# Kernel optimization log

Hardware: AMD Instinct MI355X
Metric: run time of the kernel (lower is better)

## Reference

```python
import jax, jax.numpy as jnp
import numpy as np

NUM_GROUPS = 14
GROUP_IN = 9
SHARED_H = 16
SHARED_OUT = 4
SALE_DIM = 1
FINAL_H = 128
ACTION_DIM = 15


def setup_inputs() -> dict:
    key = jax.random.key(0)
    ks = jax.random.split(key, 10)
    B = 262144
    features_2 = jax.random.normal(ks[0], (B, NUM_GROUPS * GROUP_IN), dtype=jnp.float32)
    sale_predictions = jax.random.normal(ks[1], (B, SALE_DIM), dtype=jnp.float32)
    # shared block params (one block, shared across all 14 groups)
    W1 = jax.random.normal(ks[2], (GROUP_IN, SHARED_H), dtype=jnp.float32) / np.sqrt(GROUP_IN)
    b1 = jnp.zeros((SHARED_H,), dtype=jnp.float32)
    W2 = jax.random.normal(ks[3], (SHARED_H, SHARED_OUT), dtype=jnp.float32) / np.sqrt(SHARED_H)
    b2 = jnp.zeros((SHARED_OUT,), dtype=jnp.float32)
    # final block params
    fin_in = SHARED_OUT * NUM_GROUPS + SALE_DIM  # 57
    W3 = jax.random.normal(ks[4], (fin_in, FINAL_H), dtype=jnp.float32) / np.sqrt(fin_in)
    b3 = jnp.zeros((FINAL_H,), dtype=jnp.float32)
    W4 = jax.random.normal(ks[5], (FINAL_H, ACTION_DIM * 2), dtype=jnp.float32) / np.sqrt(FINAL_H)
    b4 = jnp.zeros((ACTION_DIM * 2,), dtype=jnp.float32)
    return {"features_2": features_2, "sale_predictions": sale_predictions,
            "W1": W1, "b1": b1, "W2": W2, "b2": b2,
            "W3": W3, "b3": b3, "W4": W4, "b4": b4}


def reference(features_2, sale_predictions, W1, b1, W2, b2, W3, b3, W4, b4):
    B = features_2.shape[0]
    # [B, 14, 9]: all 14 groups through the SAME shared block, batched as one GEMM
    g = features_2.reshape(B, NUM_GROUPS, GROUP_IN)
    h = jax.nn.relu(jnp.einsum('bgi,ih->bgh', g, W1) + b1)          # [B,14,16]
    s = jax.nn.relu(jnp.einsum('bgh,ho->bgo', h, W2) + b2)          # [B,14,4]
    shared_outputs = s.reshape(B, NUM_GROUPS * SHARED_OUT)          # [B,56]
    combined = jnp.concatenate([shared_outputs, sale_predictions], axis=1)  # [B,57]
    z = jax.nn.relu(combined @ W3 + b3)                             # [B,128]
    out = z @ W4 + b4                                               # [B,30]
    action_mean, action_log_std = jnp.split(out, 2, axis=1)
    action_mean = jnp.tanh(action_mean)
    action_std = jnp.exp(action_log_std)
    return (action_mean, action_std)
```

## Files before the change

kernel.cpp:

```cpp
#include <hip/hip_runtime.h>


typedef float f4v  __attribute__((ext_vector_type(4)));
typedef short s8v  __attribute__((ext_vector_type(8)));
typedef _Float16 h8v __attribute__((ext_vector_type(8)));
typedef unsigned u2v __attribute__((ext_vector_type(2)));
typedef unsigned u4v __attribute__((ext_vector_type(4)));

constexpr int NG = 14, GI = 9, FH = 128, AD = 15;
constexpr int SLICE = 7712;

__device__ __forceinline__ unsigned short f2bf(float f) {
    unsigned u = __builtin_bit_cast(unsigned, f);
    return (unsigned short)((u + 0x7fffu + ((u >> 16) & 1u)) >> 16);
}
__device__ __forceinline__ float bf2f(unsigned short h) {
    return __builtin_bit_cast(float, (unsigned)h << 16);
}
__device__ __forceinline__ f4v load4u(const float* p) {
    f4v v; __builtin_memcpy(&v, p, 16); return v;
}
__device__ __forceinline__ unsigned pkh(float a, float b) {
    return __builtin_bit_cast(unsigned, __builtin_amdgcn_cvt_pkrtz(a, b));
}
__device__ __forceinline__ unsigned pkbf(float a, float b) {
    unsigned r;
    asm("v_cvt_pk_bf16_f32 %0, %1, %2" : "=v"(r) : "v"(a), "v"(b));
    return r;
}

__global__ void pack_kernel(const float* __restrict__ W3,
                            const float* __restrict__ W4,
                            const float* __restrict__ W1,
                            const float* __restrict__ W2,
                            unsigned short* __restrict__ pk) {
    unsigned short* W3h = pk;
    unsigned short* W3l = pk + 8192;
    unsigned short* W4h = pk + 16384;
    unsigned short* W4l = pk + 20480;
    int t = blockIdx.x * 256 + threadIdx.x;
    if (t < 8192) {
        int j = t & 7, l = (t >> 3) & 63, nt = (t >> 9) & 7, kt = t >> 12;
        int k = kt * 32 + (l >> 4) * 8 + j, n = nt * 16 + (l & 15);
        float v = (k < 57) ? W3[k * FH + n] : 0.f;
        unsigned short h = f2bf(v);
        W3h[t] = h;
        W3l[t] = f2bf(v - bf2f(h));
    }
    if (t < 4096) {
        int j = t & 7, l = (t >> 3) & 63, nt = (t >> 9) & 1, kt = t >> 10;
        int k = kt * 32 + (l >> 4) * 8 + j, n = nt * 16 + (l & 15);
        float v = (n < 30) ? W4[k * 30 + n] : 0.f;
        unsigned short h = f2bf(v);
        W4h[t] = h;
        W4l[t] = f2bf(v - bf2f(h));
    }
    if (t < 512) {
        int l = t >> 3, j = t & 7;
        int p = l >> 4, m = l & 15;
        int k = (j < 4) ? (p * 4 + j) : (16 + p * 4 + (j - 4));
        float v1 = (k < GI) ? W1[k * 16 + m] : 0.f;
        float v2 = (k < 16 && m < 4) ? W2[k * 4 + m] : 0.f;
        _Float16 h1 = (_Float16)v1, h2 = (_Float16)v2;
        pk[24576 + t] = __builtin_bit_cast(unsigned short, h1);
        pk[25088 + t] = __builtin_bit_cast(unsigned short, h2);
    }
}

__global__ __launch_bounds__(256, 4) void actor_fused(
    const float* __restrict__ x,
    const float* __restrict__ sale,
    const float* __restrict__ b1,
    const float* __restrict__ b2,
    const float* __restrict__ b3,
    const float* __restrict__ b4,
    const unsigned short* __restrict__ pk,
    float* __restrict__ om, float* __restrict__ os)
{
    __shared__ unsigned short xz[11552];
    __shared__ unsigned short sh[4096];

    const int tid  = threadIdx.x;
    const int wv   = __builtin_amdgcn_readfirstlane(tid >> 6);
    const int lane = tid & 63;
    const int row0 = blockIdx.x * 64;
    const int p    = lane >> 4;
    const int col  = lane & 15;

    {
        const float* xw0 = x + (size_t)(row0 + 16 * wv) * (NG * GI);
        #pragma unroll
        for (int i = 0; i < 4; ++i) {
            int unit = i * 64 + lane;
            if (i < 3 || lane < 32) {
                int rl = (unit * 149797) >> 21;
                int g  = unit - rl * 14;
                const float* xs = xw0 + rl * 126 + g * 9;
                f4v a = load4u(xs);
                f4v b = load4u(xs + 4);
                float c = xs[8];
                int bo = (16 * wv + rl) * 120 + g * 8;
                *(u2v*)((char*)xz + bo) = (u2v){pkh(a[0], a[1]), pkh(a[2], a[3])};
                *(u2v*)((char*)xz + SLICE + bo) = (u2v){pkh(b[0], b[1]), pkh(b[2], b[3])};
                *(u2v*)((char*)xz + 2 * SLICE + bo) = (u2v){pkh(c, 0.f), 0u};
            }
        }
    }
    if (lane < 16) {
        int r = 16 * wv + lane;
        float sv = sale[row0 + r];
        int byt = (r * 128 + 112) ^ ((r & 7) << 4);
        *(unsigned short*)((char*)sh + byt) = f2bf(sv);
        #pragma unroll
        for (int kk = 57; kk < 64; ++kk) {
            int bb = (r * 128 + kk * 2) ^ ((r & 7) << 4);
            *(unsigned short*)((char*)sh + bb) = 0;
        }
    }

    const int r1 = 16 * wv + col;
    const h8v w1t = __builtin_bit_cast(h8v, *(const s8v*)(pk + 24576 + lane * 8));
    const h8v w2t = __builtin_bit_cast(h8v, *(const s8v*)(pk + 25088 + lane * 8));
    const f4v b1f = load4u(b1 + p * 4);
    const f4v b2f = load4u(b2);
    const int psl = (p < 2) ? p : 2;
    const char* xb8 = (char*)xz + psl * SLICE + r1 * 120;
    const int sbase = r1 * 128;
    const int ssw   = (r1 & 7) << 4;

    #pragma unroll
    for (int g = 0; g < NG; ++g) {
        u2v d = *(const u2v*)(xb8 + g * 8);
        h8v xb = __builtin_bit_cast(h8v, (u4v){d[0], d[1], 0u, 0u});
        f4v ha = __builtin_amdgcn_mfma_f32_16x16x32_f16(w1t, xb, b1f, 0, 0, 0);
        float h0 = fmaxf(ha[0], 0.f), h1 = fmaxf(ha[1], 0.f);
        float h2 = fmaxf(ha[2], 0.f), h3 = fmaxf(ha[3], 0.f);
        h8v hb = __builtin_bit_cast(h8v, (u4v){pkh(h0, h1), pkh(h2, h3), 0u, 0u});
        f4v sa = __builtin_amdgcn_mfma_f32_16x16x32_f16(w2t, hb, b2f, 0, 0, 0);
        float s0 = fmaxf(sa[0], 0.f), s1 = fmaxf(sa[1], 0.f);
        float s2 = fmaxf(sa[2], 0.f), s3 = fmaxf(sa[3], 0.f);
        unsigned q0 = pkbf(s0, s1), q1 = pkbf(s2, s3);
        if (p == 0) {
            int byt = (sbase + g * 8) ^ ssw;
            *(u2v*)((char*)sh + byt) = (u2v){q0, q1};
        }
    }

    __syncthreads();

    const s8v* W3hv = (const s8v*)pk;
    const s8v* W3lv = (const s8v*)(pk + 8192);
    s8v bh[2][2], bl[2][2];
    #pragma unroll
    for (int kt = 0; kt < 2; ++kt)
        #pragma unroll
        for (int ntl = 0; ntl < 2; ++ntl) {
            int nt = 2 * wv + ntl;
            bh[kt][ntl] = W3hv[(kt * 8 + nt) * 64 + lane];
            bl[kt][ntl] = W3lv[(kt * 8 + nt) * 64 + lane];
        }
    f4v acc[4][2];
    #pragma unroll
    for (int ntl = 0; ntl < 2; ++ntl) {
        float bv = b3[32 * wv + ntl * 16 + col];
        #pragma unroll
        for (int mt = 0; mt < 4; ++mt) acc[mt][ntl] = (f4v){bv, bv, bv, bv};
    }
    #pragma unroll
    for (int kt = 0; kt < 2; ++kt) {
        s8v ah[4];
        #pragma unroll
        for (int mt = 0; mt < 4; ++mt) {
            int rr = mt * 16 + col;
            int byt = (rr * 128 + kt * 64 + p * 16) ^ ((rr & 7) << 4);
            ah[mt] = *(const s8v*)((char*)sh + byt);
        }
        #pragma unroll
        for (int mt = 0; mt < 4; ++mt)
            #pragma unroll
            for (int ntl = 0; ntl < 2; ++ntl) {
                acc[mt][ntl] = __builtin_amdgcn_mfma_f32_16x16x32_bf16(ah[mt], bh[kt][ntl], acc[mt][ntl], 0, 0, 0);
                acc[mt][ntl] = __builtin_amdgcn_mfma_f32_16x16x32_bf16(ah[mt], bl[kt][ntl], acc[mt][ntl], 0, 0, 0);
            }
    }
    #pragma unroll
    for (int mt = 0; mt < 4; ++mt)
        #pragma unroll
        for (int ntl = 0; ntl < 2; ++ntl) {
            int kk  = ntl * 16 + col;
            int tau = (kk & 4) ? 4 + (kk >> 3) : (kk >> 3);
            int eidx = mt * 2048 + wv * 512 + tau * 64 + (kk & 3) * 16 + (p << 2);
            float v0 = fmaxf(acc[mt][ntl][0], 0.f);
            float v1 = fmaxf(acc[mt][ntl][1], 0.f);
            float v2 = fmaxf(acc[mt][ntl][2], 0.f);
            float v3 = fmaxf(acc[mt][ntl][3], 0.f);
            *(u2v*)(xz + eidx) = (u2v){pkbf(v0, v1), pkbf(v2, v3)};
        }

    __syncthreads();

    const s8v* W4hv = (const s8v*)(pk + 16384);
    const s8v* W4lv = (const s8v*)(pk + 20480);
    const int mq   = __builtin_amdgcn_readfirstlane(wv >> 1);
    const int nq   = __builtin_amdgcn_readfirstlane(wv & 1);
    const int ocol = nq * 16 + col;
    const float b4i = (ocol < 30) ? b4[ocol] : 0.f;

    s8v wh[4], wl[4];
    #pragma unroll
    for (int kt = 0; kt < 4; ++kt) {
        wh[kt] = W4hv[(kt * 2 + nq) * 64 + lane];
        wl[kt] = W4lv[(kt * 2 + nq) * 64 + lane];
    }
    unsigned base = (unsigned)(size_t)&xz[0] + (unsigned)(2 * mq) * 4096u
                  + (unsigned)(lane * 8);
    u2v f0[4][2], f1[4][2];
    #pragma unroll
    for (int c = 0; c < 4; ++c) {
        unsigned a0 = base + c * 1024;
        unsigned a1 = a0 + 4096;
        asm volatile("ds_read_b64_tr_b16 %0, %1" : "=v"(f0[c][0]) : "v"(a0));
        asm volatile("ds_read_b64_tr_b16 %0, %1 offset:512" : "=v"(f0[c][1]) : "v"(a0));
        asm volatile("ds_read_b64_tr_b16 %0, %1" : "=v"(f1[c][0]) : "v"(a1));
        asm volatile("ds_read_b64_tr_b16 %0, %1 offset:512" : "=v"(f1[c][1]) : "v"(a1));
    }
    asm volatile("s_waitcnt lgkmcnt(0)" ::: "memory");
    __builtin_amdgcn_sched_barrier(0);

    f4v oa0 = (f4v){b4i, b4i, b4i, b4i};
    f4v oa1 = oa0;
    #pragma unroll
    for (int kt = 0; kt < 4; ++kt) {
        s8v z0 = __builtin_bit_cast(s8v,
            (u4v){f0[kt][0][0], f0[kt][0][1], f0[kt][1][0], f0[kt][1][1]});
        s8v z1 = __builtin_bit_cast(s8v,
            (u4v){f1[kt][0][0], f1[kt][0][1], f1[kt][1][0], f1[kt][1][1]});
        oa0 = __builtin_amdgcn_mfma_f32_16x16x32_bf16(z0, wh[kt], oa0, 0, 0, 0);
        oa0 = __builtin_amdgcn_mfma_f32_16x16x32_bf16(z0, wl[kt], oa0, 0, 0, 0);
        oa1 = __builtin_amdgcn_mfma_f32_16x16x32_bf16(z1, wh[kt], oa1, 0, 0, 0);
        oa1 = __builtin_amdgcn_mfma_f32_16x16x32_bf16(z1, wl[kt], oa1, 0, 0, 0);
    }
    #pragma unroll
    for (int mi = 0; mi < 2; ++mi) {
        f4v oa = mi ? oa1 : oa0;
        #pragma unroll
        for (int i = 0; i < 4; ++i) {
            int grow = row0 + mq * 32 + mi * 16 + p * 4 + i;
            float v = oa[i];
            if (ocol < AD) {
                float tc = fminf(fmaxf(v, -20.f), 20.f);
                float e = __expf(2.f * tc);
                om[(size_t)grow * AD + ocol] = (e - 1.f) / (e + 1.f);
            } else if (ocol < 2 * AD) {
                os[(size_t)grow * AD + (ocol - AD)] = __expf(v);
            }
        }
    }
}

extern "C" void kernel_launch(void* const* d_in, const int* in_sizes, int n_in,
                              void* d_out, int out_size, void* d_ws, size_t ws_size,
                              hipStream_t stream) {
    const float* x    = (const float*)d_in[0];
    const float* sale = (const float*)d_in[1];
    const float* W1   = (const float*)d_in[2];
    const float* b1   = (const float*)d_in[3];
    const float* W2   = (const float*)d_in[4];
    const float* b2   = (const float*)d_in[5];
    const float* W3   = (const float*)d_in[6];
    const float* b3   = (const float*)d_in[7];
    const float* W4   = (const float*)d_in[8];
    const float* b4   = (const float*)d_in[9];

    int B = in_sizes[1];
    float* om = (float*)d_out;
    float* os = om + (size_t)B * AD;
    unsigned short* pk = (unsigned short*)d_ws;

    pack_kernel<<<32, 256, 0, stream>>>(W3, W4, W1, W2, pk);
    actor_fused<<<B / 64, 256, 0, stream>>>(x, sale, b1, b2, b3, b4,
                                            pk, om, os);
}
```

Measured before the change: 49.37 us.

## Compact ninth input feature into a small LDS slice and hoist weight loads

The ninth feature of each group is now stored as a single fp16 in a compact LDS region and packed into the third dword of the MFMA B operand. W1 is repacked so that k=8 lands in the p=0 lane slot. This shrinks LDS from about 23KB to about 17.5KB per block, which may raise occupancy, and removes the padded third-slice writes. W3/b3 and W4/b4 global loads are hoisted earlier so they overlap with the input staging and the first GEMM, at the cost of more live registers.

```diff
diff --git a/kernel.cpp b/kernel.cpp
--- a/kernel.cpp
+++ b/kernel.cpp
@@ -9,6 +9,7 @@
 
 constexpr int NG = 14, GI = 9, FH = 128, AD = 15;
 constexpr int SLICE = 7712;
+constexpr int S2OFF = 15424;
 
 __device__ __forceinline__ unsigned short f2bf(float f) {
     unsigned u = __builtin_bit_cast(unsigned, f);
@@ -58,9 +59,12 @@
     if (t < 512) {
         int l = t >> 3, j = t & 7;
         int p = l >> 4, m = l & 15;
-        int k = (j < 4) ? (p * 4 + j) : (16 + p * 4 + (j - 4));
-        float v1 = (k < GI) ? W1[k * 16 + m] : 0.f;
-        float v2 = (k < 16 && m < 4) ? W2[k * 4 + m] : 0.f;
+        float v1 = 0.f;
+        if (p == 0 && j < 4)       v1 = W1[j * 16 + m];
+        else if (p == 0 && j == 4) v1 = W1[8 * 16 + m];
+        else if (p == 1 && j < 4)  v1 = W1[(4 + j) * 16 + m];
+        int k2 = (j < 4) ? (p * 4 + j) : 99;
+        float v2 = (k2 < 16 && m < 4) ? W2[k2 * 4 + m] : 0.f;
         _Float16 h1 = (_Float16)v1, h2 = (_Float16)v2;
         pk[24576 + t] = __builtin_bit_cast(unsigned short, h1);
         pk[25088 + t] = __builtin_bit_cast(unsigned short, h2);
@@ -77,7 +81,7 @@
     const unsigned short* __restrict__ pk,
     float* __restrict__ om, float* __restrict__ os)
 {
-    __shared__ unsigned short xz[11552];
+    __shared__ unsigned short xz[8736];
     __shared__ unsigned short sh[4096];
 
     const int tid  = threadIdx.x;
@@ -86,6 +90,20 @@
     const int row0 = blockIdx.x * 64;
     const int p    = lane >> 4;
     const int col  = lane & 15;
+
+    const s8v* W3hv = (const s8v*)pk;
+    const s8v* W3lv = (const s8v*)(pk + 8192);
+    s8v bh[2][2], bl[2][2];
+    #pragma unroll
+    for (int kt = 0; kt < 2; ++kt)
+        #pragma unroll
+        for (int ntl = 0; ntl < 2; ++ntl) {
+            int nt = 2 * wv + ntl;
+            bh[kt][ntl] = W3hv[(kt * 8 + nt) * 64 + lane];
+            bl[kt][ntl] = W3lv[(kt * 8 + nt) * 64 + lane];
+        }
+    const float bv0 = b3[32 * wv + col];
+    const float bv1 = b3[32 * wv + 16 + col];
 
     {
         const float* xw0 = x + (size_t)(row0 + 16 * wv) * (NG * GI);
@@ -99,10 +117,13 @@
                 f4v a = load4u(xs);
                 f4v b = load4u(xs + 4);
                 float c = xs[8];
-                int bo = (16 * wv + rl) * 120 + g * 8;
+                int r  = 16 * wv + rl;
+                int bo = r * 120 + g * 8;
                 *(u2v*)((char*)xz + bo) = (u2v){pkh(a[0], a[1]), pkh(a[2], a[3])};
                 *(u2v*)((char*)xz + SLICE + bo) = (u2v){pkh(b[0], b[1]), pkh(b[2], b[3])};
-                *(u2v*)((char*)xz + 2 * SLICE + bo) = (u2v){pkh(c, 0.f), 0u};
+                _Float16 ch = (_Float16)c;
+                *(unsigned short*)((char*)xz + S2OFF + r * 32 + g * 2) =
+                    __builtin_bit_cast(unsigned short, ch);
             }
         }
     }
@@ -123,15 +144,16 @@
     const h8v w2t = __builtin_bit_cast(h8v, *(const s8v*)(pk + 25088 + lane * 8));
     const f4v b1f = load4u(b1 + p * 4);
     const f4v b2f = load4u(b2);
-    const int psl = (p < 2) ? p : 2;
-    const char* xb8 = (char*)xz + psl * SLICE + r1 * 120;
+    const char* xb8 = (char*)xz + (p ? SLICE : 0) + r1 * 120;
+    const char* s2p = (char*)xz + S2OFF + r1 * 32;
     const int sbase = r1 * 128;
     const int ssw   = (r1 & 7) << 4;
 
     #pragma unroll
     for (int g = 0; g < NG; ++g) {
         u2v d = *(const u2v*)(xb8 + g * 8);
-        h8v xb = __builtin_bit_cast(h8v, (u4v){d[0], d[1], 0u, 0u});
+        unsigned k8 = *(const unsigned short*)(s2p + g * 2);
+        h8v xb = __builtin_bit_cast(h8v, (u4v){d[0], d[1], k8, 0u});
         f4v ha = __builtin_amdgcn_mfma_f32_16x16x32_f16(w1t, xb, b1f, 0, 0, 0);
         float h0 = fmaxf(ha[0], 0.f), h1 = fmaxf(ha[1], 0.f);
         float h2 = fmaxf(ha[2], 0.f), h3 = fmaxf(ha[3], 0.f);
@@ -148,23 +170,11 @@
 
     __syncthreads();
 
-    const s8v* W3hv = (const s8v*)pk;
-    const s8v* W3lv = (const s8v*)(pk + 8192);
-    s8v bh[2][2], bl[2][2];
-    #pragma unroll
-    for (int kt = 0; kt < 2; ++kt)
-        #pragma unroll
-        for (int ntl = 0; ntl < 2; ++ntl) {
-            int nt = 2 * wv + ntl;
-            bh[kt][ntl] = W3hv[(kt * 8 + nt) * 64 + lane];
-            bl[kt][ntl] = W3lv[(kt * 8 + nt) * 64 + lane];
-        }
     f4v acc[4][2];
     #pragma unroll
-    for (int ntl = 0; ntl < 2; ++ntl) {
-        float bv = b3[32 * wv + ntl * 16 + col];
-        #pragma unroll
-        for (int mt = 0; mt < 4; ++mt) acc[mt][ntl] = (f4v){bv, bv, bv, bv};
+    for (int mt = 0; mt < 4; ++mt) {
+        acc[mt][0] = (f4v){bv0, bv0, bv0, bv0};
+        acc[mt][1] = (f4v){bv1, bv1, bv1, bv1};
     }
     #pragma unroll
     for (int kt = 0; kt < 2; ++kt) {
@@ -183,6 +193,20 @@
                 acc[mt][ntl] = __builtin_amdgcn_mfma_f32_16x16x32_bf16(ah[mt], bl[kt][ntl], acc[mt][ntl], 0, 0, 0);
             }
     }
+
+    const s8v* W4hv = (const s8v*)(pk + 16384);
+    const s8v* W4lv = (const s8v*)(pk + 20480);
+    const int mq   = __builtin_amdgcn_readfirstlane(wv >> 1);
+    const int nq   = __builtin_amdgcn_readfirstlane(wv & 1);
+    const int ocol = nq * 16 + col;
+    s8v wh[4], wl[4];
+    #pragma unroll
+    for (int kt = 0; kt < 4; ++kt) {
+        wh[kt] = W4hv[(kt * 2 + nq) * 64 + lane];
+        wl[kt] = W4lv[(kt * 2 + nq) * 64 + lane];
+    }
+    const float b4i = (ocol < 30) ? b4[ocol] : 0.f;
+
     #pragma unroll
     for (int mt = 0; mt < 4; ++mt)
         #pragma unroll
@@ -199,19 +223,6 @@
 
     __syncthreads();
 
-    const s8v* W4hv = (const s8v*)(pk + 16384);
-    const s8v* W4lv = (const s8v*)(pk + 20480);
-    const int mq   = __builtin_amdgcn_readfirstlane(wv >> 1);
-    const int nq   = __builtin_amdgcn_readfirstlane(wv & 1);
-    const int ocol = nq * 16 + col;
-    const float b4i = (ocol < 30) ? b4[ocol] : 0.f;
-
-    s8v wh[4], wl[4];
-    #pragma unroll
-    for (int kt = 0; kt < 4; ++kt) {
-        wh[kt] = W4hv[(kt * 2 + nq) * 64 + lane];
-        wl[kt] = W4lv[(kt * 2 + nq) * 64 + lane];
-    }
     unsigned base = (unsigned)(size_t)&xz[0] + (unsigned)(2 * mq) * 4096u
                   + (unsigned)(lane * 8);
     u2v f0[4][2], f1[4][2];
```

Result: faster. 45.80 us (-7.2%).
